# Kernel optimization log

Measured on AMD Instinct MI355X. Metric: run time of the kernel, lower is better.

## Reference

```python
import jax, jax.numpy as jnp
import numpy as np

B, S, D = 16, 8192, 256
CHUNK_RATIO = 4
EPS = 1e-8  # torch F.cosine_similarity default eps


def setup_inputs() -> dict:
    key = jax.random.key(0)
    ks = jax.random.split(key, 9)
    s = 1.0 / np.sqrt(D).astype(np.float32)
    return {
        "x": jax.random.normal(ks[0], (B, S, D), jnp.float32),
        "Wq": jax.random.normal(ks[1], (D, D), jnp.float32) * s,
        "bq": jax.random.normal(ks[2], (D,), jnp.float32) * s,
        "Wk": jax.random.normal(ks[3], (D, D), jnp.float32) * s,
        "bk": jax.random.normal(ks[4], (D,), jnp.float32) * s,
        "w_vol": jax.random.normal(ks[5], (D,), jnp.float32) * s,
        "b_vol": jax.random.normal(ks[6], (1,), jnp.float32) * s,
        "w_volu": jax.random.normal(ks[7], (D,), jnp.float32) * s,
        "b_volu": jax.random.normal(ks[8], (1,), jnp.float32) * s,
    }


def reference(x, Wq, bq, Wk, bk, w_vol, b_vol, w_volu, b_volu):
    Bn, Sn, Dn = x.shape
    q = x @ Wq + bq                       # (B,S,D)
    k = x @ Wk + bk                       # (B,S,D)
    qs, kx = q[:, 1:], k[:, :-1]          # (B,S-1,D)
    dot = jnp.sum(qs * kx, axis=-1)
    sim = dot / (jnp.maximum(jnp.linalg.norm(qs, axis=-1), EPS)
                 * jnp.maximum(jnp.linalg.norm(kx, axis=-1), EPS))
    boundary_scores = 1.0 - sim           # (B,S-1)
    vol = jax.nn.sigmoid(x @ w_vol + b_vol[0])     # (B,S)
    volu = jax.nn.sigmoid(x @ w_volu + b_volu[0])  # (B,S)
    combined = jnp.concatenate(
        [jnp.ones((Bn, 1), x.dtype),
         boundary_scores + 0.3 * vol[:, 1:] + 0.2 * volu[:, 1:]], axis=1)
    boundary_probs = jax.nn.sigmoid(combined)      # (B,S)
    hard = (boundary_probs > 0.5).astype(x.dtype)  # first pos always 1 (sigmoid(1)>0.5)
    boundaries = hard + boundary_probs - jax.lax.stop_gradient(boundary_probs)
    target = jnp.asarray(Sn / CHUNK_RATIO, x.dtype)
    ratio_loss = (boundaries.sum(axis=1).mean() - target) ** 2
    # vectorized compaction: gather boundary rows to the front, zero-pad to S
    idx = jnp.cumsum(hard.astype(jnp.int32), axis=1) - 1  # destination slot per row
    brow = jnp.arange(Bn)[:, None]
    compressed = jnp.zeros((Bn, Sn, Dn), x.dtype).at[brow, idx].add(x * hard[..., None])
    return compressed, boundary_probs, ratio_loss
```

## Files before the change

### kernel.cpp

```cpp
#include <hip/hip_runtime.h>
#include <math.h>

#define BN 16
#define SN 8192
#define DN 256
#define MBLK 128
#define XROWS 129
#define EPSF 1e-8f

#define CHUNK_B 16384
#define GATE_OFF (3 * CHUNK_B)
#define LDS_BYTES (XROWS * 512)

typedef __attribute__((ext_vector_type(8))) short short8;
typedef __attribute__((ext_vector_type(4))) float f32x4;

typedef const __attribute__((address_space(1))) unsigned int g_u32;
typedef __attribute__((address_space(3))) unsigned int l_u32;

__device__ __forceinline__ unsigned short f2bf(float f) {
    union { float f; unsigned int u; } cv; cv.f = f;
    unsigned int u = cv.u + 0x7FFFu + ((cv.u >> 16) & 1u);
    return (unsigned short)(u >> 16);
}

__device__ __forceinline__ void gload_lds16(const void* g, void* l) {
    __builtin_amdgcn_global_load_lds((g_u32*)g, (l_u32*)l, 16, 0, 0);
}

__global__ void k0_prep(const float* __restrict__ Wq, const float* __restrict__ Wk,
                        const float* __restrict__ w_vol, const float* __restrict__ w_volu,
                        unsigned char* __restrict__ Wfrag, unsigned char* __restrict__ Gfrag)
{
    const int tid = threadIdx.x;
    const int n   = blockIdx.x * 8 + (tid >> 5);
    const int k8  = tid & 31;
    const int ch  = n >> 4;
    const int cc  = n & 15;
    const int ks  = k8 >> 2;
    const int g   = k8 & 3;

    short8 vq, vk;
    #pragma unroll
    for (int e = 0; e < 8; ++e) {
        const int k = k8 * 8 + e;
        vq[e] = (short)f2bf(Wq[(size_t)k * DN + n]);
        vk[e] = (short)f2bf(Wk[(size_t)k * DN + n]);
    }
    const size_t base = (size_t)ch * CHUNK_B + (size_t)((g * 16 + cc) * 16);
    *(short8*)(Wfrag + base + (size_t)(ks)     * 1024) = vq;
    *(short8*)(Wfrag + base + (size_t)(8 + ks) * 1024) = vk;

    if (blockIdx.x < 2) {
        const int gc = blockIdx.x * 8 + (tid >> 5);
        short8 vg;
        #pragma unroll
        for (int e = 0; e < 8; ++e) {
            const int k = k8 * 8 + e;
            float v = (gc == 0) ? w_vol[k] : ((gc == 1) ? w_volu[k] : 0.0f);
            vg[e] = (short)f2bf(v);
        }
        *(short8*)(Gfrag + (size_t)ks * 1024 + (size_t)((g * 16 + gc) * 16)) = vg;
    }
}

__global__ __launch_bounds__(256, 2) void k1_mfma(
    const float* __restrict__ x,
    const unsigned char* __restrict__ Wfrag,
    const unsigned char* __restrict__ Gfrag,
    const float* __restrict__ bq, const float* __restrict__ bk,
    const float* __restrict__ b_vol, const float* __restrict__ b_volu,
    float* __restrict__ bp_out, int* __restrict__ flags)
{
    extern __shared__ unsigned char lds[];

    const int tid = threadIdx.x;
    const int wm  = tid >> 6;
    const int l   = tid & 63;
    const int g   = l >> 4;
    const int c   = l & 15;
    const int b   = blockIdx.y;
    const int s0  = blockIdx.x * MBLK;

    {
        unsigned short* xs = (unsigned short*)lds;
        const float* xb = x + (size_t)b * SN * DN;
        for (int f = tid; f < XROWS * 32; f += 256) {
            const int row = f >> 5, ch = f & 31;
            const int gs = s0 - 1 + row;
            float v[8];
            if (gs >= 0) {
                const float4* p = (const float4*)(xb + (size_t)gs * DN + ch * 8);
                float4 a = p[0], d = p[1];
                v[0] = a.x; v[1] = a.y; v[2] = a.z; v[3] = a.w;
                v[4] = d.x; v[5] = d.y; v[6] = d.z; v[7] = d.w;
            } else {
                #pragma unroll
                for (int i = 0; i < 8; ++i) v[i] = 0.0f;
            }
            short8 sv;
            #pragma unroll
            for (int i = 0; i < 8; ++i) sv[i] = (short)f2bf(v[i]);
            const int byte = row * 512 + ((ch * 16) ^ ((row & 7) << 4));
            *(short8*)((char*)xs + byte) = sv;
        }
    }
    __syncthreads();

    short8 aq[2][8], ak[2][8];
    #pragma unroll
    for (int m = 0; m < 2; ++m) {
        const int rk = wm * 32 + m * 16 + c;
        const int rq = rk + 1;
        #pragma unroll
        for (int ks = 0; ks < 8; ++ks) {
            const int oq = rq * 512 + (((ks * 64) + g * 16) ^ ((rq & 7) << 4));
            const int ok = rk * 512 + (((ks * 64) + g * 16) ^ ((rk & 7) << 4));
            aq[m][ks] = *(const short8*)((const char*)lds + oq);
            ak[m][ks] = *(const short8*)((const char*)lds + ok);
        }
    }
    __syncthreads();

    float bqv[16], bkv[16];
    #pragma unroll
    for (int i = 0; i < 16; ++i) { bqv[i] = bq[i * 16 + c]; bkv[i] = bk[i * 16 + c]; }

    {
        #pragma unroll
        for (int j = 0; j < 4; ++j)
            gload_lds16(Wfrag + j * 4096 + tid * 16, lds + j * 4096 + wm * 1024);
        #pragma unroll
        for (int j = 0; j < 2; ++j)
            gload_lds16(Gfrag + j * 4096 + tid * 16, lds + GATE_OFF + j * 4096 + wm * 1024);
        #pragma unroll
        for (int j = 0; j < 4; ++j)
            gload_lds16(Wfrag + CHUNK_B + j * 4096 + tid * 16, lds + CHUNK_B + j * 4096 + wm * 1024);
    }
    asm volatile("s_waitcnt vmcnt(4)" ::: "memory");
    __builtin_amdgcn_s_barrier();

    float dt[2][4], nqv[2][4], nkv[2][4];
    #pragma unroll
    for (int m = 0; m < 2; ++m)
        #pragma unroll
        for (int r = 0; r < 4; ++r) { dt[m][r] = 0.f; nqv[m][r] = 0.f; nkv[m][r] = 0.f; }

    #pragma unroll
    for (int i = 0; i < 16; ++i) {
        if (i + 2 <= 15) {
            const unsigned char* src = Wfrag + (size_t)(i + 2) * CHUNK_B;
            unsigned char* dst = lds + ((i + 2) % 3) * CHUNK_B;
            #pragma unroll
            for (int j = 0; j < 4; ++j)
                gload_lds16(src + j * 4096 + tid * 16, dst + j * 4096 + wm * 1024);
        }

        const unsigned char* bb = lds + (i % 3) * CHUNK_B;
        f32x4 cq[2], ck[2];
        cq[0] = (f32x4)(0.f); cq[1] = (f32x4)(0.f);
        ck[0] = (f32x4)(0.f); ck[1] = (f32x4)(0.f);
        #pragma unroll
        for (int ks = 0; ks < 8; ++ks) {
            const short8 bqf = *(const short8*)(bb + ks * 1024 + l * 16);
            const short8 bkf = *(const short8*)(bb + (8 + ks) * 1024 + l * 16);
            cq[0] = __builtin_amdgcn_mfma_f32_16x16x32_bf16(aq[0][ks], bqf, cq[0], 0, 0, 0);
            cq[1] = __builtin_amdgcn_mfma_f32_16x16x32_bf16(aq[1][ks], bqf, cq[1], 0, 0, 0);
            ck[0] = __builtin_amdgcn_mfma_f32_16x16x32_bf16(ak[0][ks], bkf, ck[0], 0, 0, 0);
            ck[1] = __builtin_amdgcn_mfma_f32_16x16x32_bf16(ak[1][ks], bkf, ck[1], 0, 0, 0);
        }

        #pragma unroll
        for (int m = 0; m < 2; ++m)
            #pragma unroll
            for (int r = 0; r < 4; ++r) {
                const float qv = cq[m][r] + bqv[i];
                const float kv = ck[m][r] + bkv[i];
                dt[m][r]  = fmaf(qv, kv, dt[m][r]);
                nqv[m][r] = fmaf(qv, qv, nqv[m][r]);
                nkv[m][r] = fmaf(kv, kv, nkv[m][r]);
            }

        if (i + 2 <= 15) asm volatile("s_waitcnt vmcnt(4)" ::: "memory");
        else             asm volatile("s_waitcnt vmcnt(0)" ::: "memory");
        __builtin_amdgcn_s_barrier();
    }

    f32x4 cg[2];
    cg[0] = (f32x4)(0.f); cg[1] = (f32x4)(0.f);
    #pragma unroll
    for (int ks = 0; ks < 8; ++ks) {
        const short8 bgf = *(const short8*)(lds + GATE_OFF + ks * 1024 + l * 16);
        cg[0] = __builtin_amdgcn_mfma_f32_16x16x32_bf16(aq[0][ks], bgf, cg[0], 0, 0, 0);
        cg[1] = __builtin_amdgcn_mfma_f32_16x16x32_bf16(aq[1][ks], bgf, cg[1], 0, 0, 0);
    }

    #pragma unroll
    for (int m = 0; m < 2; ++m)
        #pragma unroll
        for (int r = 0; r < 4; ++r) {
            float a = dt[m][r], e = nqv[m][r], f = nkv[m][r];
            #pragma unroll
            for (int mask = 1; mask < 16; mask <<= 1) {
                a += __shfl_xor(a, mask);
                e += __shfl_xor(e, mask);
                f += __shfl_xor(f, mask);
            }
            dt[m][r] = a; nqv[m][r] = e; nkv[m][r] = f;
        }
    float vu_[2][4];
    #pragma unroll
    for (int m = 0; m < 2; ++m)
        #pragma unroll
        for (int r = 0; r < 4; ++r) vu_[m][r] = __shfl_xor(cg[m][r], 1);

    if (c == 0) {
        const float bv = b_vol[0], bu = b_volu[0];
        #pragma unroll
        for (int m = 0; m < 2; ++m)
            #pragma unroll
            for (int r = 0; r < 4; ++r) {
                const int s = s0 + wm * 32 + m * 16 + g * 4 + r;
                float comb;
                if (s == 0) comb = 1.0f;
                else {
                    float denom = fmaxf(sqrtf(nqv[m][r]), EPSF) * fmaxf(sqrtf(nkv[m][r]), EPSF);
                    float sim   = dt[m][r] / denom;
                    float vol   = 1.f / (1.f + expf(-(cg[m][r] + bv)));
                    float volu  = 1.f / (1.f + expf(-(vu_[m][r] + bu)));
                    comb = (1.f - sim) + 0.3f * vol + 0.2f * volu;
                }
                const float pbp = 1.f / (1.f + expf(-comb));
                const size_t o = (size_t)b * SN + s;
                bp_out[o] = pbp;
                flags[o]  = (pbp > 0.5f) ? 1 : 0;
            }
    }
}

__global__ void k2_scan(const int* __restrict__ flags,
                        const float* __restrict__ bp,
                        int* __restrict__ pidx,
                        int* __restrict__ cnt,
                        float* __restrict__ bsum)
{
    const int b = blockIdx.x;
    const int t = threadIdx.x;
    __shared__ int   ssum[256];
    __shared__ float sf[256];

    const size_t base = (size_t)b * SN + (size_t)t * 32;
    int f[32];
    int run = 0;
    float fs = 0.f;
    #pragma unroll
    for (int i = 0; i < 32; ++i) {
        f[i] = flags[base + i];
        run += f[i];
        float p  = bp[base + i];
        float hf = (float)f[i];
        fs += hf + p - p;
    }
    ssum[t] = run;
    sf[t]   = fs;
    __syncthreads();

    for (int off = 1; off < 256; off <<= 1) {
        int v = (t >= off) ? ssum[t - off] : 0;
        __syncthreads();
        ssum[t] += v;
        __syncthreads();
    }
    const int incl = ssum[t];
    int running = incl - run;
    #pragma unroll
    for (int i = 0; i < 32; ++i) {
        running += f[i];
        pidx[base + i] = f[i] ? (running - 1) : -1;
    }
    if (t == 255) cnt[b] = incl;

    for (int off = 128; off > 0; off >>= 1) {
        if (t < off) sf[t] += sf[t + off];
        __syncthreads();
    }
    if (t == 0) bsum[b] = sf[0];
}

__global__ void k3_scatter(const float* __restrict__ x,
                           const int* __restrict__ pidx,
                           float* __restrict__ out_comp)
{
    const int row  = blockIdx.x * 4 + (threadIdx.x >> 6);
    const int lane = threadIdx.x & 63;
    const int p = pidx[row];
    if (p < 0) return;
    const int b = row >> 13;
    const float4* src = (const float4*)(x + (size_t)row * DN);
    float4* dst = (float4*)(out_comp + ((size_t)b * SN + p) * DN);
    dst[lane] = src[lane];
}

__global__ void k3b_zerotail(float* __restrict__ out_comp,
                             const int* __restrict__ cnt)
{
    const int gid = blockIdx.x * blockDim.x + threadIdx.x;
    const int b = gid >> 13;
    const int j = gid & (SN - 1);
    if (j >= cnt[b]) {
        float4* dst = (float4*)(out_comp + ((size_t)b * SN + j) * DN);
        const float4 z = make_float4(0.f, 0.f, 0.f, 0.f);
        for (int i = 0; i < DN / 4; ++i) dst[i] = z;
    }
}

__global__ void k4_loss(const float* __restrict__ bsum, float* __restrict__ out_rl)
{
    if (threadIdx.x == 0) {
        float acc = 0.f;
        for (int i = 0; i < BN; ++i) acc += bsum[i];
        float mean = acc / (float)BN;
        float d = mean - (float)(SN / 4);
        out_rl[0] = d * d;
    }
}

extern "C" void kernel_launch(void* const* d_in, const int* in_sizes, int n_in,
                              void* d_out, int out_size, void* d_ws, size_t ws_size,
                              hipStream_t stream) {
    const float* x      = (const float*)d_in[0];
    const float* Wq     = (const float*)d_in[1];
    const float* bq     = (const float*)d_in[2];
    const float* Wk     = (const float*)d_in[3];
    const float* bk     = (const float*)d_in[4];
    const float* w_vol  = (const float*)d_in[5];
    const float* b_vol  = (const float*)d_in[6];
    const float* w_volu = (const float*)d_in[7];
    const float* b_volu = (const float*)d_in[8];

    float* out_comp = (float*)d_out;
    float* out_bp   = out_comp + (size_t)BN * SN * DN;
    float* out_rl   = out_bp + (size_t)BN * SN;

    int*   flags = (int*)d_ws;
    int*   pidx  = flags + (size_t)BN * SN;
    int*   cnt   = pidx + (size_t)BN * SN;
    float* bsum  = (float*)(cnt + BN);
    unsigned char* Wfrag = (unsigned char*)(bsum + BN);
    unsigned char* Gfrag = Wfrag + 262144;

    k0_prep<<<32, 256, 0, stream>>>(Wq, Wk, w_vol, w_volu, Wfrag, Gfrag);

    hipFuncSetAttribute((const void*)k1_mfma,
                        hipFuncAttributeMaxDynamicSharedMemorySize, LDS_BYTES);

    k1_mfma<<<dim3(SN / MBLK, BN), 256, LDS_BYTES, stream>>>(
        x, Wfrag, Gfrag, bq, bk, b_vol, b_volu, out_bp, flags);

    k2_scan<<<BN, 256, 0, stream>>>(flags, out_bp, pidx, cnt, bsum);

    k3_scatter<<<(BN * SN) / 4, 256, 0, stream>>>(x, pidx, out_comp);

    k3b_zerotail<<<(BN * SN) / 256, 256, 0, stream>>>(out_comp, cnt);

    k4_loss<<<1, 64, 0, stream>>>(bsum, out_rl);
}
```

Before: 118.4 us.

## Share A fragments for Q and K, shift K via shuffles, precompute tile-boundary K rows

The MFMA kernel now keeps one set of bf16 A fragments per row instead of separate Q and K fragments, which halves register use and the size of the x staging buffer. The one-row shift for the K rows is done with cross-lane shuffles, and a new pre-kernel computes K for the row just before each 32-row wave tile in fp32. x is staged through a double-buffered 32-row LDS region, and the gate weights become a 17th chunk in the streamed weight pipeline. LDS drops to 48KB and launch bounds rise to 3 blocks per CU for more occupancy, at the cost of an extra kernel launch and mixed precision at the boundary rows.

```diff
diff --git a/kernel.cpp b/kernel.cpp
--- a/kernel.cpp
+++ b/kernel.cpp
@@ -5,12 +5,11 @@
 #define SN 8192
 #define DN 256
 #define MBLK 128
-#define XROWS 129
 #define EPSF 1e-8f
 
 #define CHUNK_B 16384
-#define GATE_OFF (3 * CHUNK_B)
-#define LDS_BYTES (XROWS * 512)
+#define NCHUNK 17
+#define LDS_BYTES (3 * CHUNK_B)
 
 typedef __attribute__((ext_vector_type(8))) short short8;
 typedef __attribute__((ext_vector_type(4))) float f32x4;
@@ -30,7 +29,7 @@
 
 __global__ void k0_prep(const float* __restrict__ Wq, const float* __restrict__ Wk,
                         const float* __restrict__ w_vol, const float* __restrict__ w_volu,
-                        unsigned char* __restrict__ Wfrag, unsigned char* __restrict__ Gfrag)
+                        unsigned char* __restrict__ Wfrag)
 {
     const int tid = threadIdx.x;
     const int n   = blockIdx.x * 8 + (tid >> 5);
@@ -51,6 +50,7 @@
     *(short8*)(Wfrag + base + (size_t)(ks)     * 1024) = vq;
     *(short8*)(Wfrag + base + (size_t)(8 + ks) * 1024) = vk;
 
+    unsigned char* Gfrag = Wfrag + (size_t)16 * CHUNK_B;
     if (blockIdx.x < 2) {
         const int gc = blockIdx.x * 8 + (tid >> 5);
         short8 vg;
@@ -61,82 +61,114 @@
             vg[e] = (short)f2bf(v);
         }
         *(short8*)(Gfrag + (size_t)ks * 1024 + (size_t)((g * 16 + gc) * 16)) = vg;
-    }
-}
-
-__global__ __launch_bounds__(256, 2) void k1_mfma(
+    } else if (blockIdx.x < 4) {
+        short8 z = (short8)(0);
+        *(short8*)(Gfrag + 8192 + (size_t)(blockIdx.x - 2) * 4096 + (size_t)tid * 16) = z;
+    }
+}
+
+__global__ void k0b_kpatch(const float* __restrict__ x, const float* __restrict__ Wk,
+                           float* __restrict__ kpatch)
+{
+    __shared__ float xr[8][DN];
+    const int b  = blockIdx.y;
+    const int r0 = blockIdx.x * 8;
+    const int t  = threadIdx.x;
+    #pragma unroll
+    for (int m = 0; m < 8; ++m)
+        xr[m][t] = x[((size_t)b * SN + 31 + (size_t)(r0 + m) * 32) * DN + t];
+    __syncthreads();
+    float acc[8];
+    #pragma unroll
+    for (int m = 0; m < 8; ++m) acc[m] = 0.f;
+    #pragma unroll 4
+    for (int k = 0; k < DN; ++k) {
+        const float w = Wk[(size_t)k * DN + t];
+        #pragma unroll
+        for (int m = 0; m < 8; ++m) acc[m] = fmaf(xr[m][k], w, acc[m]);
+    }
+    #pragma unroll
+    for (int m = 0; m < 8; ++m)
+        kpatch[((size_t)b * 256 + r0 + m) * DN + t] = acc[m];
+}
+
+__global__ __launch_bounds__(256, 3) void k1_mfma(
     const float* __restrict__ x,
     const unsigned char* __restrict__ Wfrag,
-    const unsigned char* __restrict__ Gfrag,
+    const float* __restrict__ kpatch,
     const float* __restrict__ bq, const float* __restrict__ bk,
     const float* __restrict__ b_vol, const float* __restrict__ b_volu,
     float* __restrict__ bp_out, int* __restrict__ flags)
 {
     extern __shared__ unsigned char lds[];
 
-    const int tid = threadIdx.x;
-    const int wm  = tid >> 6;
-    const int l   = tid & 63;
-    const int g   = l >> 4;
-    const int c   = l & 15;
-    const int b   = blockIdx.y;
-    const int s0  = blockIdx.x * MBLK;
+    const int tid  = threadIdx.x;
+    const int wq   = tid >> 6;
+    const int l    = tid & 63;
+    const int g    = l >> 4;
+    const int c    = l & 15;
+    const int b    = blockIdx.y;
+    const int blkx = blockIdx.x;
+    const int s0   = blkx * MBLK;
+
+    const float* xb = x + (size_t)b * SN * DN;
 
     {
-        unsigned short* xs = (unsigned short*)lds;
-        const float* xb = x + (size_t)b * SN * DN;
-        for (int f = tid; f < XROWS * 32; f += 256) {
-            const int row = f >> 5, ch = f & 31;
-            const int gs = s0 - 1 + row;
-            float v[8];
-            if (gs >= 0) {
-                const float4* p = (const float4*)(xb + (size_t)gs * DN + ch * 8);
-                float4 a = p[0], d = p[1];
-                v[0] = a.x; v[1] = a.y; v[2] = a.z; v[3] = a.w;
-                v[4] = d.x; v[5] = d.y; v[6] = d.z; v[7] = d.w;
-            } else {
+        unsigned char* reg = lds;
+        #pragma unroll
+        for (int it = 0; it < 4; ++it) {
+            const int f = it * 256 + tid;
+            const int rho = f >> 5, ch = f & 31;
+            const float4* p = (const float4*)(xb + (size_t)(s0 + rho) * DN + ch * 8);
+            const float4 aa = p[0], dd = p[1];
+            short8 sv;
+            sv[0] = (short)f2bf(aa.x); sv[1] = (short)f2bf(aa.y);
+            sv[2] = (short)f2bf(aa.z); sv[3] = (short)f2bf(aa.w);
+            sv[4] = (short)f2bf(dd.x); sv[5] = (short)f2bf(dd.y);
+            sv[6] = (short)f2bf(dd.z); sv[7] = (short)f2bf(dd.w);
+            *(short8*)(reg + rho * 512 + ((ch * 16) ^ ((rho & 7) << 4))) = sv;
+        }
+    }
+    __syncthreads();
+
+    short8 a[2][8];
+    #pragma unroll
+    for (int qt = 0; qt < 4; ++qt) {
+        if (qt < 3) {
+            unsigned char* reg = lds + ((qt + 1) & 1) * CHUNK_B;
+            #pragma unroll
+            for (int it = 0; it < 4; ++it) {
+                const int f = it * 256 + tid;
+                const int rho = f >> 5, ch = f & 31;
+                const float4* p = (const float4*)(xb + (size_t)(s0 + (qt + 1) * 32 + rho) * DN + ch * 8);
+                const float4 aa = p[0], dd = p[1];
+                short8 sv;
+                sv[0] = (short)f2bf(aa.x); sv[1] = (short)f2bf(aa.y);
+                sv[2] = (short)f2bf(aa.z); sv[3] = (short)f2bf(aa.w);
+                sv[4] = (short)f2bf(dd.x); sv[5] = (short)f2bf(dd.y);
+                sv[6] = (short)f2bf(dd.z); sv[7] = (short)f2bf(dd.w);
+                *(short8*)(reg + rho * 512 + ((ch * 16) ^ ((rho & 7) << 4))) = sv;
+            }
+        }
+        if (wq == qt) {
+            const unsigned char* reg = lds + (qt & 1) * CHUNK_B;
+            #pragma unroll
+            for (int m = 0; m < 2; ++m) {
+                const int rho = m * 16 + c;
                 #pragma unroll
-                for (int i = 0; i < 8; ++i) v[i] = 0.0f;
-            }
-            short8 sv;
-            #pragma unroll
-            for (int i = 0; i < 8; ++i) sv[i] = (short)f2bf(v[i]);
-            const int byte = row * 512 + ((ch * 16) ^ ((row & 7) << 4));
-            *(short8*)((char*)xs + byte) = sv;
-        }
-    }
-    __syncthreads();
-
-    short8 aq[2][8], ak[2][8];
-    #pragma unroll
-    for (int m = 0; m < 2; ++m) {
-        const int rk = wm * 32 + m * 16 + c;
-        const int rq = rk + 1;
-        #pragma unroll
-        for (int ks = 0; ks < 8; ++ks) {
-            const int oq = rq * 512 + (((ks * 64) + g * 16) ^ ((rq & 7) << 4));
-            const int ok = rk * 512 + (((ks * 64) + g * 16) ^ ((rk & 7) << 4));
-            aq[m][ks] = *(const short8*)((const char*)lds + oq);
-            ak[m][ks] = *(const short8*)((const char*)lds + ok);
-        }
-    }
-    __syncthreads();
-
-    float bqv[16], bkv[16];
-    #pragma unroll
-    for (int i = 0; i < 16; ++i) { bqv[i] = bq[i * 16 + c]; bkv[i] = bk[i * 16 + c]; }
-
-    {
-        #pragma unroll
-        for (int j = 0; j < 4; ++j)
-            gload_lds16(Wfrag + j * 4096 + tid * 16, lds + j * 4096 + wm * 1024);
-        #pragma unroll
-        for (int j = 0; j < 2; ++j)
-            gload_lds16(Gfrag + j * 4096 + tid * 16, lds + GATE_OFF + j * 4096 + wm * 1024);
-        #pragma unroll
-        for (int j = 0; j < 4; ++j)
-            gload_lds16(Wfrag + CHUNK_B + j * 4096 + tid * 16, lds + CHUNK_B + j * 4096 + wm * 1024);
-    }
+                for (int ks = 0; ks < 8; ++ks)
+                    a[m][ks] = *(const short8*)(reg + rho * 512 + (((ks * 64) + g * 16) ^ ((rho & 7) << 4)));
+            }
+        }
+        __syncthreads();
+    }
+
+    #pragma unroll
+    for (int j = 0; j < 4; ++j)
+        gload_lds16(Wfrag + j * 4096 + tid * 16, lds + j * 4096 + wq * 1024);
+    #pragma unroll
+    for (int j = 0; j < 4; ++j)
+        gload_lds16(Wfrag + CHUNK_B + j * 4096 + tid * 16, lds + CHUNK_B + j * 4096 + wq * 1024);
     asm volatile("s_waitcnt vmcnt(4)" ::: "memory");
     __builtin_amdgcn_s_barrier();
 
@@ -145,74 +177,88 @@
     for (int m = 0; m < 2; ++m)
         #pragma unroll
         for (int r = 0; r < 4; ++r) { dt[m][r] = 0.f; nqv[m][r] = 0.f; nkv[m][r] = 0.f; }
-
-    #pragma unroll
-    for (int i = 0; i < 16; ++i) {
-        if (i + 2 <= 15) {
+    f32x4 cg0 = (f32x4)(0.f), cg1 = (f32x4)(0.f);
+
+    int kpidx = 4 * blkx + wq - 1;
+    if (kpidx < 0) kpidx = 0;
+    const float* kpp = kpatch + ((size_t)b * 256 + kpidx) * DN;
+
+    #pragma unroll
+    for (int i = 0; i < NCHUNK; ++i) {
+        if (i + 2 < NCHUNK) {
             const unsigned char* src = Wfrag + (size_t)(i + 2) * CHUNK_B;
             unsigned char* dst = lds + ((i + 2) % 3) * CHUNK_B;
             #pragma unroll
             for (int j = 0; j < 4; ++j)
-                gload_lds16(src + j * 4096 + tid * 16, dst + j * 4096 + wm * 1024);
-        }
-
+                gload_lds16(src + j * 4096 + tid * 16, dst + j * 4096 + wq * 1024);
+        }
         const unsigned char* bb = lds + (i % 3) * CHUNK_B;
-        f32x4 cq[2], ck[2];
-        cq[0] = (f32x4)(0.f); cq[1] = (f32x4)(0.f);
-        ck[0] = (f32x4)(0.f); ck[1] = (f32x4)(0.f);
-        #pragma unroll
-        for (int ks = 0; ks < 8; ++ks) {
-            const short8 bqf = *(const short8*)(bb + ks * 1024 + l * 16);
-            const short8 bkf = *(const short8*)(bb + (8 + ks) * 1024 + l * 16);
-            cq[0] = __builtin_amdgcn_mfma_f32_16x16x32_bf16(aq[0][ks], bqf, cq[0], 0, 0, 0);
-            cq[1] = __builtin_amdgcn_mfma_f32_16x16x32_bf16(aq[1][ks], bqf, cq[1], 0, 0, 0);
-            ck[0] = __builtin_amdgcn_mfma_f32_16x16x32_bf16(ak[0][ks], bkf, ck[0], 0, 0, 0);
-            ck[1] = __builtin_amdgcn_mfma_f32_16x16x32_bf16(ak[1][ks], bkf, ck[1], 0, 0, 0);
-        }
-
-        #pragma unroll
-        for (int m = 0; m < 2; ++m)
+
+        if (i < 16) {
+            f32x4 cq0 = (f32x4)(0.f), cq1 = (f32x4)(0.f);
+            f32x4 ck0 = (f32x4)(0.f), ck1 = (f32x4)(0.f);
+            #pragma unroll
+            for (int ks = 0; ks < 8; ++ks) {
+                const short8 bqf = *(const short8*)(bb + ks * 1024 + l * 16);
+                const short8 bkf = *(const short8*)(bb + (8 + ks) * 1024 + l * 16);
+                cq0 = __builtin_amdgcn_mfma_f32_16x16x32_bf16(a[0][ks], bqf, cq0, 0, 0, 0);
+                cq1 = __builtin_amdgcn_mfma_f32_16x16x32_bf16(a[1][ks], bqf, cq1, 0, 0, 0);
+                ck0 = __builtin_amdgcn_mfma_f32_16x16x32_bf16(a[0][ks], bkf, ck0, 0, 0, 0);
+                ck1 = __builtin_amdgcn_mfma_f32_16x16x32_bf16(a[1][ks], bkf, ck1, 0, 0, 0);
+            }
+            const float bqc = bq[i * 16 + c];
+            const float bkc = bk[i * 16 + c];
+            const float kb  = kpp[i * 16 + c];
+            const float sh0 = __shfl(ck0[3], (l - 16) & 63);
+            const float sh1 = __shfl(ck1[3], (l - 16) & 63);
+            const float cr  = __shfl(ck0[3], 48 + c);
+            const float km00 = (g == 0) ? kb : sh0;
+            const float km10 = (g == 0) ? cr : sh1;
+            const float kv0[4] = {km00, ck0[0], ck0[1], ck0[2]};
+            const float kv1[4] = {km10, ck1[0], ck1[1], ck1[2]};
             #pragma unroll
             for (int r = 0; r < 4; ++r) {
-                const float qv = cq[m][r] + bqv[i];
-                const float kv = ck[m][r] + bkv[i];
-                dt[m][r]  = fmaf(qv, kv, dt[m][r]);
-                nqv[m][r] = fmaf(qv, qv, nqv[m][r]);
-                nkv[m][r] = fmaf(kv, kv, nkv[m][r]);
-            }
-
-        if (i + 2 <= 15) asm volatile("s_waitcnt vmcnt(4)" ::: "memory");
-        else             asm volatile("s_waitcnt vmcnt(0)" ::: "memory");
+                float qv = cq0[r] + bqc;
+                float kv = kv0[r] + bkc;
+                dt[0][r]  = fmaf(qv, kv, dt[0][r]);
+                nqv[0][r] = fmaf(qv, qv, nqv[0][r]);
+                nkv[0][r] = fmaf(kv, kv, nkv[0][r]);
+                qv = cq1[r] + bqc;
+                kv = kv1[r] + bkc;
+                dt[1][r]  = fmaf(qv, kv, dt[1][r]);
+                nqv[1][r] = fmaf(qv, qv, nqv[1][r]);
+                nkv[1][r] = fmaf(kv, kv, nkv[1][r]);
+            }
+        } else {
+            #pragma unroll
+            for (int ks = 0; ks < 8; ++ks) {
+                const short8 bgf = *(const short8*)(bb + ks * 1024 + l * 16);
+                cg0 = __builtin_amdgcn_mfma_f32_16x16x32_bf16(a[0][ks], bgf, cg0, 0, 0, 0);
+                cg1 = __builtin_amdgcn_mfma_f32_16x16x32_bf16(a[1][ks], bgf, cg1, 0, 0, 0);
+            }
+        }
+
+        if (i < NCHUNK - 2) asm volatile("s_waitcnt vmcnt(4)" ::: "memory");
+        else                asm volatile("s_waitcnt vmcnt(0)" ::: "memory");
         __builtin_amdgcn_s_barrier();
     }
 
-    f32x4 cg[2];
-    cg[0] = (f32x4)(0.f); cg[1] = (f32x4)(0.f);
-    #pragma unroll
-    for (int ks = 0; ks < 8; ++ks) {
-        const short8 bgf = *(const short8*)(lds + GATE_OFF + ks * 1024 + l * 16);
-        cg[0] = __builtin_amdgcn_mfma_f32_16x16x32_bf16(aq[0][ks], bgf, cg[0], 0, 0, 0);
-        cg[1] = __builtin_amdgcn_mfma_f32_16x16x32_bf16(aq[1][ks], bgf, cg[1], 0, 0, 0);
-    }
-
     #pragma unroll
     for (int m = 0; m < 2; ++m)
         #pragma unroll
         for (int r = 0; r < 4; ++r) {
-            float a = dt[m][r], e = nqv[m][r], f = nkv[m][r];
+            float aa = dt[m][r], e = nqv[m][r], f = nkv[m][r];
             #pragma unroll
             for (int mask = 1; mask < 16; mask <<= 1) {
-                a += __shfl_xor(a, mask);
-                e += __shfl_xor(e, mask);
-                f += __shfl_xor(f, mask);
-            }
-            dt[m][r] = a; nqv[m][r] = e; nkv[m][r] = f;
-        }
-    float vu_[2][4];
-    #pragma unroll
-    for (int m = 0; m < 2; ++m)
-        #pragma unroll
-        for (int r = 0; r < 4; ++r) vu_[m][r] = __shfl_xor(cg[m][r], 1);
+                aa += __shfl_xor(aa, mask);
+                e  += __shfl_xor(e, mask);
+                f  += __shfl_xor(f, mask);
+            }
+            dt[m][r] = aa; nqv[m][r] = e; nkv[m][r] = f;
+        }
+    float vu0[4], vu1[4];
+    #pragma unroll
+    for (int r = 0; r < 4; ++r) { vu0[r] = __shfl_xor(cg0[r], 1); vu1[r] = __shfl_xor(cg1[r], 1); }
 
     if (c == 0) {
         const float bv = b_vol[0], bu = b_volu[0];
@@ -220,14 +266,16 @@
         for (int m = 0; m < 2; ++m)
             #pragma unroll
             for (int r = 0; r < 4; ++r) {
-                const int s = s0 + wm * 32 + m * 16 + g * 4 + r;
+                const int s = s0 + wq * 32 + m * 16 + g * 4 + r;
+                const float cgv = (m == 0) ? cg0[r] : cg1[r];
+                const float vuv = (m == 0) ? vu0[r] : vu1[r];
                 float comb;
                 if (s == 0) comb = 1.0f;
                 else {
                     float denom = fmaxf(sqrtf(nqv[m][r]), EPSF) * fmaxf(sqrtf(nkv[m][r]), EPSF);
                     float sim   = dt[m][r] / denom;
-                    float vol   = 1.f / (1.f + expf(-(cg[m][r] + bv)));
-                    float volu  = 1.f / (1.f + expf(-(vu_[m][r] + bu)));
+                    float vol   = 1.f / (1.f + expf(-(cgv + bv)));
+                    float volu  = 1.f / (1.f + expf(-(vuv + bu)));
                     comb = (1.f - sim) + 0.3f * vol + 0.2f * volu;
                 }
                 const float pbp = 1.f / (1.f + expf(-comb));
@@ -347,15 +395,17 @@
     int*   cnt   = pidx + (size_t)BN * SN;
     float* bsum  = (float*)(cnt + BN);
     unsigned char* Wfrag = (unsigned char*)(bsum + BN);
-    unsigned char* Gfrag = Wfrag + 262144;
-
-    k0_prep<<<32, 256, 0, stream>>>(Wq, Wk, w_vol, w_volu, Wfrag, Gfrag);
+    float* kpatch = (float*)(Wfrag + (size_t)NCHUNK * CHUNK_B);
+
+    k0_prep<<<32, 256, 0, stream>>>(Wq, Wk, w_vol, w_volu, Wfrag);
+
+    k0b_kpatch<<<dim3(32, BN), 256, 0, stream>>>(x, Wk, kpatch);
 
     hipFuncSetAttribute((const void*)k1_mfma,
                         hipFuncAttributeMaxDynamicSharedMemorySize, LDS_BYTES);
 
     k1_mfma<<<dim3(SN / MBLK, BN), 256, LDS_BYTES, stream>>>(
-        x, Wfrag, Gfrag, bq, bk, b_vol, b_volu, out_bp, flags);
+        x, Wfrag, kpatch, bq, bk, b_vol, b_volu, out_bp, flags);
 
     k2_scan<<<BN, 256, 0, stream>>>(flags, out_bp, pidx, cnt, bsum);
 
```

New measurement: 139.4 us. 17.7% more time.
